# Optimization experiments

Hardware: AMD Instinct MI355X
Metric: run time of the kernel (lower is better)

The kernel has to match this reference:

```python
import jax, jax.numpy as jnp
import numpy as np

N_NODES = 50000


def setup_inputs() -> dict:
    key = jax.random.key(0)
    ks = jax.random.split(key, 10)
    B, N, D, H, O = 2, N_NODES, 128, 128, 10
    x = jax.random.normal(ks[0], (B, N, D), dtype=jnp.float32)
    edge_index = jax.random.randint(ks[1], (2, 800000), 0, N, dtype=jnp.int32)
    s = lambda fan_in: 1.0 / np.sqrt(fan_in)
    W  = jax.random.uniform(ks[2], (D, H), jnp.float32, -s(D), s(D))
    b  = jnp.zeros((H,), jnp.float32)
    W1 = jax.random.uniform(ks[3], (H, H // 2), jnp.float32, -s(H), s(H))
    b1 = jnp.zeros((H // 2,), jnp.float32)
    W2 = jax.random.uniform(ks[4], (H // 2, H // 4), jnp.float32, -s(H // 2), s(H // 2))
    b2 = jnp.zeros((H // 4,), jnp.float32)
    W3 = jax.random.uniform(ks[5], (H // 4, O), jnp.float32, -s(H // 4), s(H // 4))
    b3 = jnp.zeros((O,), jnp.float32)
    return {"x": x, "edge_index": edge_index, "W": W, "b": b,
            "W1": W1, "b1": b1, "W2": W2, "b2": b2, "W3": W3, "b3": b3}


def reference(x, edge_index, W, b, W1, b1, W2, b2, W3, b3):
    # GraphConvolution (Kipf): support = x @ W; out[dst] += support[src]; + b
    src, dst = edge_index[0], edge_index[1]
    support = jnp.einsum("bnd,dh->bnh", x, W)          # [B, N, H]
    msgs = support[:, src, :]                            # [B, E, H] gather
    agg = jnp.zeros_like(support).at[:, dst, :].add(msgs)  # scatter-add
    h = jax.nn.gelu(agg + b, approximate=False)          # GELU (torch default erf)
    # dropout is identity at inference (training=False)
    h = jax.nn.relu(jnp.einsum("bnh,hk->bnk", h, W1) + b1)
    h = jax.nn.relu(jnp.einsum("bnk,km->bnm", h, W2) + b2)
    h = jnp.einsum("bnm,mo->bno", h, W3) + b3            # [B, N, O]
    return h.mean(axis=1)                                # [B, O]
```

## Files before the change

kernel.cpp:

```cpp
#include <hip/hip_runtime.h>
#include <math.h>

#define NN 50000
#define DD 128
#define HH 128
#define L1 64
#define L2 32
#define OO 10

typedef short v8s __attribute__((ext_vector_type(8)));
typedef float v4f __attribute__((ext_vector_type(4)));

__device__ __forceinline__ float bf2f_lo(unsigned u) { return __uint_as_float(u << 16); }
__device__ __forceinline__ float bf2f_hi(unsigned u) { return __uint_as_float(u & 0xffff0000u); }
__device__ __forceinline__ unsigned short f2bf(float f) {
    unsigned u = __float_as_uint(f);
    return (unsigned short)((u + 0x7fffu + ((u >> 16) & 1u)) >> 16);
}
__device__ __forceinline__ float gelu_f(float v) {
    return 0.5f * v * (1.f + erff(v * 0.70710678118654752f));
}

__global__ __launch_bounds__(256) void k_wprep(
    const float* __restrict__ W, unsigned short* __restrict__ wtb)
{
    int i = blockIdx.x * 256 + threadIdx.x;
    if (i < 128 * 136) {
        int n = i / 136, k = i % 136;
        wtb[i] = (k < DD) ? f2bf(W[k * HH + n]) : (unsigned short)0;
    }
}

__global__ __launch_bounds__(256) void k_support(
    const float* __restrict__ x, const unsigned short* __restrict__ wtb,
    unsigned short* __restrict__ supb, int rows,
    const int* __restrict__ ei, int* __restrict__ counts, int E)
{
    __shared__ __align__(16) unsigned short xs[64 * 136];
    __shared__ __align__(16) unsigned short wt[128 * 136];
    const int tid = threadIdx.x;
    const int row0 = blockIdx.x * 64;

    for (int u = tid * 4; u < 128 * 136; u += 1024)
        *(uint2*)(&wt[u]) = *(const uint2*)(wtb + u);
    for (int u = tid * 4; u < 64 * DD; u += 1024) {
        const int r = u >> 7, c = u & 127;
        float4 v = make_float4(0.f, 0.f, 0.f, 0.f);
        if (row0 + r < rows) v = *(const float4*)(x + (size_t)(row0 + r) * DD + c);
        ushort4 o;
        o.x = f2bf(v.x); o.y = f2bf(v.y); o.z = f2bf(v.z); o.w = f2bf(v.w);
        *(ushort4*)(&xs[r * 136 + c]) = o;
    }

    {
        const int chunk = (E + gridDim.x - 1) / gridDim.x;
        const int e0 = blockIdx.x * chunk;
        const int e1 = min(e0 + chunk, E);
        for (int e = e0 + tid; e < e1; e += 256)
            atomicAdd(&counts[ei[(size_t)E + e]], 1);
    }
    __syncthreads();

    const int lane = tid & 63;
    const int w = tid >> 6;
    const int m0 = w * 16;
    const int lm = lane & 15;
    const int q  = lane >> 4;

    v4f acc[8];
    #pragma unroll
    for (int i = 0; i < 8; ++i) acc[i] = (v4f)(0.f);

    #pragma unroll
    for (int ks = 0; ks < 4; ++ks) {
        const int k0 = ks * 32 + q * 8;
        const v8s af = *(const v8s*)(&xs[(m0 + lm) * 136 + k0]);
        #pragma unroll
        for (int ct = 0; ct < 8; ++ct) {
            const v8s bf = *(const v8s*)(&wt[(ct * 16 + lm) * 136 + k0]);
            acc[ct] = __builtin_amdgcn_mfma_f32_16x16x32_bf16(af, bf, acc[ct], 0, 0, 0);
        }
    }

    #pragma unroll
    for (int ct = 0; ct < 8; ++ct) {
        const int col = ct * 16 + lm;
        #pragma unroll
        for (int r = 0; r < 4; ++r) {
            const int rowg = row0 + m0 + q * 4 + r;
            if (rowg < rows) {
                const int b = (rowg >= NN) ? 1 : 0;
                const int n = rowg - b * NN;
                supb[((size_t)n * 2 + b) * HH + col] = f2bf(acc[ct][r]);
            }
        }
    }
}

__global__ __launch_bounds__(1024) void k_scan1(
    const int* __restrict__ counts, int* __restrict__ offsets,
    int* __restrict__ blksum, int n)
{
    __shared__ int wsum[16], woff[16];
    const int tid = threadIdx.x, lane = tid & 63, wv = tid >> 6;
    const int i = blockIdx.x * 1024 + tid;
    int v = (i < n) ? counts[i] : 0;
    int x = v;
    #pragma unroll
    for (int d = 1; d < 64; d <<= 1) { int t = __shfl_up(x, d); if (lane >= d) x += t; }
    if (lane == 63) wsum[wv] = x;
    __syncthreads();
    if (wv == 0 && lane < 16) {
        int y = wsum[lane];
        #pragma unroll
        for (int d = 1; d < 16; d <<= 1) { int t = __shfl_up(y, d); if (lane >= d) y += t; }
        woff[lane] = y - wsum[lane];
        if (lane == 15) blksum[blockIdx.x] = y;
    }
    __syncthreads();
    if (i < n) offsets[i] = woff[wv] + (x - v);
}

__global__ __launch_bounds__(1024) void k_scan2(
    int* __restrict__ offsets, const int* __restrict__ blksum, int nblk, int n)
{
    __shared__ int base_sh, tot_sh;
    const int tid = threadIdx.x, lane = tid & 63, wv = tid >> 6;
    if (wv == 0) {
        int v = (lane < nblk) ? blksum[lane] : 0;
        int x = v;
        #pragma unroll
        for (int d = 1; d < 64; d <<= 1) { int t = __shfl_up(x, d); if (lane >= d) x += t; }
        int incl = __shfl(x, blockIdx.x);
        int own  = __shfl(v, blockIdx.x);
        int tot  = __shfl(x, nblk - 1);
        if (lane == 0) { base_sh = incl - own; tot_sh = tot; }
    }
    __syncthreads();
    const int i = blockIdx.x * 1024 + tid;
    if (i < n) offsets[i] += base_sh;
    if (blockIdx.x == nblk - 1 && tid == 0) offsets[n] = tot_sh;
}

__global__ __launch_bounds__(256) void k_bucket(
    const int* __restrict__ ei, const int* __restrict__ offsets,
    int* __restrict__ cursor, int* __restrict__ ss, int E)
{
    int e = blockIdx.x * 256 + threadIdx.x;
    if (e < E) {
        int d = ei[E + e];
        int pos = offsets[d] + atomicAdd(&cursor[d], 1);
        ss[pos] = ei[e];
    }
}

__global__ __launch_bounds__(256) void k_agg(
    const unsigned short* __restrict__ supb, const int* __restrict__ offsets,
    const int* __restrict__ ss, unsigned short* __restrict__ aggb, int nn)
{
    const int tid = threadIdx.x;
    const int lane = tid & 63;
    const int wv = tid >> 6;
    const int d = blockIdx.x * 4 + wv;
    if (d >= nn) return;
    const unsigned short* sp = supb + lane * 4;
    const int s0 = offsets[d], s1 = offsets[d + 1];
    float4 a = make_float4(0.f, 0.f, 0.f, 0.f);
    float4 a2 = make_float4(0.f, 0.f, 0.f, 0.f);
    int i = s0;
    for (; i + 4 <= s1; i += 4) {
        const int sA = ss[i], sB = ss[i + 1], sC = ss[i + 2], sD = ss[i + 3];
        const uint2 rA = *(const uint2*)(sp + (size_t)sA * 256);
        const uint2 rB = *(const uint2*)(sp + (size_t)sB * 256);
        const uint2 rC = *(const uint2*)(sp + (size_t)sC * 256);
        const uint2 rD = *(const uint2*)(sp + (size_t)sD * 256);
        a.x  += bf2f_lo(rA.x); a.y  += bf2f_hi(rA.x); a.z  += bf2f_lo(rA.y); a.w  += bf2f_hi(rA.y);
        a2.x += bf2f_lo(rB.x); a2.y += bf2f_hi(rB.x); a2.z += bf2f_lo(rB.y); a2.w += bf2f_hi(rB.y);
        a.x  += bf2f_lo(rC.x); a.y  += bf2f_hi(rC.x); a.z  += bf2f_lo(rC.y); a.w  += bf2f_hi(rC.y);
        a2.x += bf2f_lo(rD.x); a2.y += bf2f_hi(rD.x); a2.z += bf2f_lo(rD.y); a2.w += bf2f_hi(rD.y);
    }
    for (; i < s1; ++i) {
        const uint2 r = *(const uint2*)(sp + (size_t)ss[i] * 256);
        a.x += bf2f_lo(r.x); a.y += bf2f_hi(r.x); a.z += bf2f_lo(r.y); a.w += bf2f_hi(r.y);
    }
    a.x += a2.x; a.y += a2.y; a.z += a2.z; a.w += a2.w;
    ushort4 o;
    o.x = f2bf(a.x); o.y = f2bf(a.y); o.z = f2bf(a.z); o.w = f2bf(a.w);
    *(ushort4*)(aggb + (size_t)d * 256 + lane * 4) = o;
}

__global__ __launch_bounds__(512) void k_mlp(
    const unsigned short* __restrict__ aggb, const float* __restrict__ b0v,
    const float* __restrict__ W1, const float* __restrict__ b1v,
    const float* __restrict__ W2, const float* __restrict__ b2v,
    float* __restrict__ partials, int srows)
{
    __shared__ float w1s[HH][L1];
    __shared__ float w2s[L1][L2];
    __shared__ float hs[64 * 136];
    __shared__ float b0s[DD], b1s[L1], b2s[L2];
    __shared__ float oacc[64];

    const int tid = threadIdx.x;
    const int row0 = blockIdx.x * 64;

    for (int u = tid * 4; u < HH * L1; u += 2048)
        *(float4*)(&w1s[u >> 6][u & 63]) = *(const float4*)(W1 + u);
    for (int u = tid * 4; u < L1 * L2; u += 2048)
        *(float4*)(&w2s[u >> 5][u & 31]) = *(const float4*)(W2 + u);
    if (tid < DD) b0s[tid] = b0v[tid];
    if (tid < L1) b1s[tid] = b1v[tid];
    if (tid < L2) b2s[tid] = b2v[tid];
    if (tid < 64) oacc[tid] = 0.f;
    __syncthreads();

    for (int u = tid * 8; u < 64 * DD; u += 512 * 8) {
        const int r = u >> 7, c = u & 127;
        float4 g0 = make_float4(0.f, 0.f, 0.f, 0.f);
        float4 g1 = g0;
        if (row0 + r < srows) {
            const uint4 raw = *(const uint4*)(aggb + (size_t)(row0 + r) * HH + c);
            float v[8];
            v[0] = bf2f_lo(raw.x) + b0s[c + 0]; v[1] = bf2f_hi(raw.x) + b0s[c + 1];
            v[2] = bf2f_lo(raw.y) + b0s[c + 2]; v[3] = bf2f_hi(raw.y) + b0s[c + 3];
            v[4] = bf2f_lo(raw.z) + b0s[c + 4]; v[5] = bf2f_hi(raw.z) + b0s[c + 5];
            v[6] = bf2f_lo(raw.w) + b0s[c + 6]; v[7] = bf2f_hi(raw.w) + b0s[c + 7];
            #pragma unroll
            for (int t = 0; t < 8; ++t) v[t] = gelu_f(v[t]);
            g0 = make_float4(v[0], v[1], v[2], v[3]);
            g1 = make_float4(v[4], v[5], v[6], v[7]);
        }
        *(float4*)(&hs[r * 136 + c]) = g0;
        *(float4*)(&hs[r * 136 + c + 4]) = g1;
    }
    __syncthreads();

    const int cg = tid & 15;
    const int rg = tid >> 4;
    float4 acc0 = *(const float4*)(&b1s[cg * 4]);
    float4 acc1 = acc0;
    #pragma unroll 4
    for (int j = 0; j < HH; j += 4) {
        float4 wv[4];
        #pragma unroll
        for (int jj = 0; jj < 4; ++jj) wv[jj] = *(const float4*)(&w1s[j + jj][cg * 4]);
        const float4 h0 = *(const float4*)(&hs[(rg * 2 + 0) * 136 + j]);
        const float4 h1 = *(const float4*)(&hs[(rg * 2 + 1) * 136 + j]);
        acc0.x = fmaf(h0.x, wv[0].x, fmaf(h0.y, wv[1].x, fmaf(h0.z, wv[2].x, fmaf(h0.w, wv[3].x, acc0.x))));
        acc0.y = fmaf(h0.x, wv[0].y, fmaf(h0.y, wv[1].y, fmaf(h0.z, wv[2].y, fmaf(h0.w, wv[3].y, acc0.y))));
        acc0.z = fmaf(h0.x, wv[0].z, fmaf(h0.y, wv[1].z, fmaf(h0.z, wv[2].z, fmaf(h0.w, wv[3].z, acc0.z))));
        acc0.w = fmaf(h0.x, wv[0].w, fmaf(h0.y, wv[1].w, fmaf(h0.z, wv[2].w, fmaf(h0.w, wv[3].w, acc0.w))));
        acc1.x = fmaf(h1.x, wv[0].x, fmaf(h1.y, wv[1].x, fmaf(h1.z, wv[2].x, fmaf(h1.w, wv[3].x, acc1.x))));
        acc1.y = fmaf(h1.x, wv[0].y, fmaf(h1.y, wv[1].y, fmaf(h1.z, wv[2].y, fmaf(h1.w, wv[3].y, acc1.y))));
        acc1.z = fmaf(h1.x, wv[0].z, fmaf(h1.y, wv[1].z, fmaf(h1.z, wv[2].z, fmaf(h1.w, wv[3].z, acc1.z))));
        acc1.w = fmaf(h1.x, wv[0].w, fmaf(h1.y, wv[1].w, fmaf(h1.z, wv[2].w, fmaf(h1.w, wv[3].w, acc1.w))));
    }
    acc0.x = fmaxf(acc0.x, 0.f); acc0.y = fmaxf(acc0.y, 0.f);
    acc0.z = fmaxf(acc0.z, 0.f); acc0.w = fmaxf(acc0.w, 0.f);
    acc1.x = fmaxf(acc1.x, 0.f); acc1.y = fmaxf(acc1.y, 0.f);
    acc1.z = fmaxf(acc1.z, 0.f); acc1.w = fmaxf(acc1.w, 0.f);
    __syncthreads();
    float* h1p = hs;
    *(float4*)(&h1p[(rg * 2 + 0) * 68 + cg * 4]) = acc0;
    *(float4*)(&h1p[(rg * 2 + 1) * 68 + cg * 4]) = acc1;
    __syncthreads();

    float* h2p = hs + 5120;
    {
        const int cg2 = tid & 7;
        const int r2 = tid >> 3;
        float4 a = *(const float4*)(&b2s[cg2 * 4]);
        #pragma unroll 4
        for (int j = 0; j < L1; j += 4) {
            float4 wv[4];
            #pragma unroll
            for (int jj = 0; jj < 4; ++jj) wv[jj] = *(const float4*)(&w2s[j + jj][cg2 * 4]);
            const float4 hv = *(const float4*)(&h1p[r2 * 68 + j]);
            a.x = fmaf(hv.x, wv[0].x, fmaf(hv.y, wv[1].x, fmaf(hv.z, wv[2].x, fmaf(hv.w, wv[3].x, a.x))));
            a.y = fmaf(hv.x, wv[0].y, fmaf(hv.y, wv[1].y, fmaf(hv.z, wv[2].y, fmaf(hv.w, wv[3].y, a.y))));
            a.z = fmaf(hv.x, wv[0].z, fmaf(hv.y, wv[1].z, fmaf(hv.z, wv[2].z, fmaf(hv.w, wv[3].z, a.z))));
            a.w = fmaf(hv.x, wv[0].w, fmaf(hv.y, wv[1].w, fmaf(hv.z, wv[2].w, fmaf(hv.w, wv[3].w, a.w))));
        }
        a.x = fmaxf(a.x, 0.f); a.y = fmaxf(a.y, 0.f);
        a.z = fmaxf(a.z, 0.f); a.w = fmaxf(a.w, 0.f);
        __syncthreads();
        *(float4*)(&h2p[r2 * 36 + cg2 * 4]) = a;
    }
    __syncthreads();

    {
        const int c = tid & 31;
        const int g = tid >> 5;
        float p0 = 0.f, p1 = 0.f;
        #pragma unroll
        for (int i = 0; i < 4; ++i) {
            const int r = g * 4 + i;
            if (row0 + r < srows) {
                const float v = h2p[r * 36 + c];
                if (r & 1) p1 += v; else p0 += v;
            }
        }
        if (p0 != 0.f) atomicAdd(&oacc[c], p0);
        if (p1 != 0.f) atomicAdd(&oacc[32 + c], p1);
    }
    __syncthreads();
    if (tid < 64) partials[(size_t)blockIdx.x * 64 + tid] = oacc[tid];
}

__global__ __launch_bounds__(256) void k_scatter(
    const int* __restrict__ ei, const unsigned short* __restrict__ supb,
    float* __restrict__ aggf, int E)
{
    const int tid = threadIdx.x;
    const int eg = tid >> 6;
    const int lane = tid & 63;
    const int e = blockIdx.x * 4 + eg;
    if (e >= E) return;
    const int src = ei[e];
    const int dst = ei[E + e];
    const uint2 r = *(const uint2*)(supb + (size_t)src * 256 + lane * 4);
    float* ap = aggf + (size_t)dst * 256 + lane * 4;
    unsafeAtomicAdd(ap + 0, bf2f_lo(r.x));
    unsafeAtomicAdd(ap + 1, bf2f_hi(r.x));
    unsafeAtomicAdd(ap + 2, bf2f_lo(r.y));
    unsafeAtomicAdd(ap + 3, bf2f_hi(r.y));
}

__global__ __launch_bounds__(256) void k_cvt(
    const float* __restrict__ in, unsigned short* __restrict__ outb, int n)
{
    int i = blockIdx.x * 256 + threadIdx.x;
    if (i < n) outb[i] = f2bf(in[i]);
}

__global__ __launch_bounds__(256) void k_reduce(
    const float* __restrict__ partials, float* __restrict__ accum, int nblk)
{
    __shared__ float lsum[4][64];
    const int t = threadIdx.x & 63;
    const int w = threadIdx.x >> 6;
    float s = 0.f;
    for (int g = blockIdx.x * 4 + w; g < nblk; g += gridDim.x * 4)
        s += partials[(size_t)g * 64 + t];
    lsum[w][t] = s;
    __syncthreads();
    if (threadIdx.x < 64) {
        const float v = lsum[0][t] + lsum[1][t] + lsum[2][t] + lsum[3][t];
        unsafeAtomicAdd(&accum[t], v);
    }
}

__global__ __launch_bounds__(64) void k_final(
    const float* __restrict__ accum, const float* __restrict__ W3,
    const float* __restrict__ b3v, float* __restrict__ out)
{
    const int tid = threadIdx.x;
    if (tid < 2 * OO) {
        const int b = tid / OO, o = tid % OO;
        float acc = b3v[o];
        const float inv = 1.0f / (float)NN;
        #pragma unroll
        for (int j = 0; j < L2; ++j) acc += (accum[b * 32 + j] * inv) * W3[j * OO + o];
        out[tid] = acc;
    }
}

extern "C" void kernel_launch(void* const* d_in, const int* in_sizes, int n_in,
                              void* d_out, int out_size, void* d_ws, size_t ws_size,
                              hipStream_t stream) {
    const float* x  = (const float*)d_in[0];
    const int*   ei = (const int*)d_in[1];
    const float* W  = (const float*)d_in[2];
    const float* b0 = (const float*)d_in[3];
    const float* W1 = (const float*)d_in[4];
    const float* b1 = (const float*)d_in[5];
    const float* W2 = (const float*)d_in[6];
    const float* b2 = (const float*)d_in[7];
    const float* W3 = (const float*)d_in[8];
    const float* b3 = (const float*)d_in[9];
    float* out = (float*)d_out;

    const int E = in_sizes[1] / 2;
    const int rows = 2 * NN;
    const int nblk = (rows + 63) / 64;
    const int nsb = (NN + 1023) / 1024;

    unsigned short* supb = (unsigned short*)d_ws;
    unsigned short* aggb = supb + (size_t)rows * HH;
    float* partials = (float*)(aggb + (size_t)rows * HH);
    float* accum    = partials + (size_t)nblk * 64;
    int*   counts   = (int*)(accum + 64);
    int*   cursor   = counts + NN;
    int*   offsets  = cursor + NN;
    int*   blksum   = offsets + NN + 1;
    unsigned short* wtb = (unsigned short*)(blksum + 64);
    int*   ss       = (int*)(wtb + 128 * 136);
    float* aggf     = (float*)(ss + E);
    const size_t need_csr = ((size_t)rows * HH * 2 + 128 * 136) * sizeof(unsigned short)
                      + ((size_t)nblk * 64 + 64) * sizeof(float)
                      + ((size_t)NN * 3 + 1 + 64 + E) * sizeof(int);
    const size_t need_fb = need_csr + (size_t)rows * HH * sizeof(float);

    if (ws_size >= need_csr && nsb <= 64) {
        hipMemsetAsync(accum, 0, (64 + 2 * (size_t)NN) * sizeof(int), stream);
        k_wprep<<<dim3((128 * 136 + 255) / 256), dim3(256), 0, stream>>>(W, wtb);
        k_support<<<dim3((rows + 63) / 64), dim3(256), 0, stream>>>(x, wtb, supb, rows, ei, counts, E);
        k_scan1<<<dim3(nsb), dim3(1024), 0, stream>>>(counts, offsets, blksum, NN);
        k_scan2<<<dim3(nsb), dim3(1024), 0, stream>>>(offsets, blksum, nsb, NN);
        k_bucket<<<dim3((E + 255) / 256), dim3(256), 0, stream>>>(ei, offsets, cursor, ss, E);
        k_agg<<<dim3((NN + 3) / 4), dim3(256), 0, stream>>>(supb, offsets, ss, aggb, NN);
        k_mlp<<<dim3(nblk), dim3(512), 0, stream>>>(aggb, b0, W1, b1, W2, b2, partials, rows);
    } else if (ws_size >= need_fb) {
        hipMemsetAsync(accum, 0, 64 * sizeof(float), stream);
        hipMemsetAsync(aggf, 0, (size_t)rows * HH * sizeof(float), stream);
        k_wprep<<<dim3((128 * 136 + 255) / 256), dim3(256), 0, stream>>>(W, wtb);
        k_support<<<dim3((rows + 63) / 64), dim3(256), 0, stream>>>(x, wtb, supb, rows, ei, counts, 0);
        k_scatter<<<dim3((E + 3) / 4), dim3(256), 0, stream>>>(ei, supb, aggf, E);
        k_cvt<<<dim3((rows * HH + 255) / 256), dim3(256), 0, stream>>>(aggf, aggb, rows * HH);
        k_mlp<<<dim3(nblk), dim3(512), 0, stream>>>(aggb, b0, W1, b1, W2, b2, partials, rows);
    }

    k_reduce<<<dim3(64), dim3(256), 0, stream>>>(partials, accum, nblk);
    k_final<<<dim3(1), dim3(64), 0, stream>>>(accum, W3, b3, out);
}
```

Before: 310.2 us.

## Use bf16 MFMA for MLP layers and enlarge support-GEMM tiles

The two MLP layers (128→64, 64→32) in k_mlp now run on bf16 MFMA instructions instead of scalar fp32 FMAs. The weights are pre-transposed and converted to bf16 in k_wprep, and the GELU activations and layer-1 outputs are stored as bf16 in shared memory. Separately, k_support now uses 128-row tiles with 512 threads, so each block amortises the shared weight load over more rows. This adds bf16 rounding of the intermediate activations and weights, and the larger support tile uses more LDS per block, which may lower occupancy.

```diff
diff --git a/kernel.cpp b/kernel.cpp
--- a/kernel.cpp
+++ b/kernel.cpp
@@ -22,28 +22,38 @@
 }
 
 __global__ __launch_bounds__(256) void k_wprep(
-    const float* __restrict__ W, unsigned short* __restrict__ wtb)
+    const float* __restrict__ W, const float* __restrict__ W1,
+    const float* __restrict__ W2, unsigned short* __restrict__ wtb,
+    unsigned short* __restrict__ w1tb, unsigned short* __restrict__ w2tb)
 {
     int i = blockIdx.x * 256 + threadIdx.x;
     if (i < 128 * 136) {
         int n = i / 136, k = i % 136;
         wtb[i] = (k < DD) ? f2bf(W[k * HH + n]) : (unsigned short)0;
-    }
-}
-
-__global__ __launch_bounds__(256) void k_support(
+    } else if (i < 128 * 136 + 64 * 136) {
+        int j = i - 128 * 136;
+        int n = j / 136, k = j % 136;
+        w1tb[j] = (k < HH) ? f2bf(W1[k * L1 + n]) : (unsigned short)0;
+    } else if (i < 128 * 136 + 64 * 136 + 32 * 72) {
+        int j = i - (128 * 136 + 64 * 136);
+        int n = j / 72, k = j % 72;
+        w2tb[j] = (k < L1) ? f2bf(W2[k * L2 + n]) : (unsigned short)0;
+    }
+}
+
+__global__ __launch_bounds__(512, 4) void k_support(
     const float* __restrict__ x, const unsigned short* __restrict__ wtb,
     unsigned short* __restrict__ supb, int rows,
     const int* __restrict__ ei, int* __restrict__ counts, int E)
 {
-    __shared__ __align__(16) unsigned short xs[64 * 136];
+    __shared__ __align__(16) unsigned short xs[128 * 136];
     __shared__ __align__(16) unsigned short wt[128 * 136];
     const int tid = threadIdx.x;
-    const int row0 = blockIdx.x * 64;
-
-    for (int u = tid * 4; u < 128 * 136; u += 1024)
+    const int row0 = blockIdx.x * 128;
+
+    for (int u = tid * 4; u < 128 * 136; u += 2048)
         *(uint2*)(&wt[u]) = *(const uint2*)(wtb + u);
-    for (int u = tid * 4; u < 64 * DD; u += 1024) {
+    for (int u = tid * 4; u < 128 * DD; u += 2048) {
         const int r = u >> 7, c = u & 127;
         float4 v = make_float4(0.f, 0.f, 0.f, 0.f);
         if (row0 + r < rows) v = *(const float4*)(x + (size_t)(row0 + r) * DD + c);
@@ -56,7 +66,7 @@
         const int chunk = (E + gridDim.x - 1) / gridDim.x;
         const int e0 = blockIdx.x * chunk;
         const int e1 = min(e0 + chunk, E);
-        for (int e = e0 + tid; e < e1; e += 256)
+        for (int e = e0 + tid; e < e1; e += 512)
             atomicAdd(&counts[ei[(size_t)E + e]], 1);
     }
     __syncthreads();
@@ -189,102 +199,98 @@
     *(ushort4*)(aggb + (size_t)d * 256 + lane * 4) = o;
 }
 
-__global__ __launch_bounds__(512) void k_mlp(
+__global__ __launch_bounds__(512, 6) void k_mlp(
     const unsigned short* __restrict__ aggb, const float* __restrict__ b0v,
-    const float* __restrict__ W1, const float* __restrict__ b1v,
-    const float* __restrict__ W2, const float* __restrict__ b2v,
+    const unsigned short* __restrict__ w1tb, const float* __restrict__ b1v,
+    const unsigned short* __restrict__ w2tb, const float* __restrict__ b2v,
     float* __restrict__ partials, int srows)
 {
-    __shared__ float w1s[HH][L1];
-    __shared__ float w2s[L1][L2];
-    __shared__ float hs[64 * 136];
+    __shared__ __align__(16) unsigned short wt1[64 * 136];
+    __shared__ __align__(16) unsigned short wt2[32 * 72];
+    __shared__ __align__(16) unsigned char upool[64 * 136 * 2];
+    __shared__ __align__(16) unsigned short h1b[64 * 72];
     __shared__ float b0s[DD], b1s[L1], b2s[L2];
     __shared__ float oacc[64];
+    unsigned short* hsb = (unsigned short*)upool;
+    float* h2p = (float*)upool;
 
     const int tid = threadIdx.x;
     const int row0 = blockIdx.x * 64;
 
-    for (int u = tid * 4; u < HH * L1; u += 2048)
-        *(float4*)(&w1s[u >> 6][u & 63]) = *(const float4*)(W1 + u);
-    for (int u = tid * 4; u < L1 * L2; u += 2048)
-        *(float4*)(&w2s[u >> 5][u & 31]) = *(const float4*)(W2 + u);
+    for (int u = tid * 4; u < 64 * 136; u += 2048)
+        *(uint2*)(&wt1[u]) = *(const uint2*)(w1tb + u);
+    for (int u = tid * 4; u < 32 * 72; u += 2048)
+        *(uint2*)(&wt2[u]) = *(const uint2*)(w2tb + u);
     if (tid < DD) b0s[tid] = b0v[tid];
     if (tid < L1) b1s[tid] = b1v[tid];
     if (tid < L2) b2s[tid] = b2v[tid];
     if (tid < 64) oacc[tid] = 0.f;
-    __syncthreads();
-
-    for (int u = tid * 8; u < 64 * DD; u += 512 * 8) {
+
+    for (int u = tid * 8; u < 64 * DD; u += 4096) {
         const int r = u >> 7, c = u & 127;
-        float4 g0 = make_float4(0.f, 0.f, 0.f, 0.f);
-        float4 g1 = g0;
-        if (row0 + r < srows) {
-            const uint4 raw = *(const uint4*)(aggb + (size_t)(row0 + r) * HH + c);
-            float v[8];
-            v[0] = bf2f_lo(raw.x) + b0s[c + 0]; v[1] = bf2f_hi(raw.x) + b0s[c + 1];
-            v[2] = bf2f_lo(raw.y) + b0s[c + 2]; v[3] = bf2f_hi(raw.y) + b0s[c + 3];
-            v[4] = bf2f_lo(raw.z) + b0s[c + 4]; v[5] = bf2f_hi(raw.z) + b0s[c + 5];
-            v[6] = bf2f_lo(raw.w) + b0s[c + 6]; v[7] = bf2f_hi(raw.w) + b0s[c + 7];
+        uint4 raw = make_uint4(0, 0, 0, 0);
+        if (row0 + r < srows) raw = *(const uint4*)(aggb + (size_t)(row0 + r) * HH + c);
+        float v[8];
+        v[0] = bf2f_lo(raw.x) + b0s[c + 0]; v[1] = bf2f_hi(raw.x) + b0s[c + 1];
+        v[2] = bf2f_lo(raw.y) + b0s[c + 2]; v[3] = bf2f_hi(raw.y) + b0s[c + 3];
+        v[4] = bf2f_lo(raw.z) + b0s[c + 4]; v[5] = bf2f_hi(raw.z) + b0s[c + 5];
+        v[6] = bf2f_lo(raw.w) + b0s[c + 6]; v[7] = bf2f_hi(raw.w) + b0s[c + 7];
+        ushort4 o0, o1;
+        o0.x = f2bf(gelu_f(v[0])); o0.y = f2bf(gelu_f(v[1]));
+        o0.z = f2bf(gelu_f(v[2])); o0.w = f2bf(gelu_f(v[3]));
+        o1.x = f2bf(gelu_f(v[4])); o1.y = f2bf(gelu_f(v[5]));
+        o1.z = f2bf(gelu_f(v[6])); o1.w = f2bf(gelu_f(v[7]));
+        *(ushort4*)(&hsb[r * 136 + c]) = o0;
+        *(ushort4*)(&hsb[r * 136 + c + 4]) = o1;
+    }
+    __syncthreads();
+
+    const int lane = tid & 63;
+    const int w = tid >> 6;
+    const int lm = lane & 15;
+    const int q = lane >> 4;
+    const int r1 = (w & 3) * 16;
+
+    {
+        const int c1 = (w >> 2) * 32;
+        v4f a1[2];
+        a1[0] = (v4f)(0.f); a1[1] = (v4f)(0.f);
+        #pragma unroll
+        for (int ks = 0; ks < 4; ++ks) {
+            const int k0 = ks * 32 + q * 8;
+            const v8s af = *(const v8s*)(&hsb[(r1 + lm) * 136 + k0]);
             #pragma unroll
-            for (int t = 0; t < 8; ++t) v[t] = gelu_f(v[t]);
-            g0 = make_float4(v[0], v[1], v[2], v[3]);
-            g1 = make_float4(v[4], v[5], v[6], v[7]);
-        }
-        *(float4*)(&hs[r * 136 + c]) = g0;
-        *(float4*)(&hs[r * 136 + c + 4]) = g1;
-    }
-    __syncthreads();
-
-    const int cg = tid & 15;
-    const int rg = tid >> 4;
-    float4 acc0 = *(const float4*)(&b1s[cg * 4]);
-    float4 acc1 = acc0;
-    #pragma unroll 4
-    for (int j = 0; j < HH; j += 4) {
-        float4 wv[4];
-        #pragma unroll
-        for (int jj = 0; jj < 4; ++jj) wv[jj] = *(const float4*)(&w1s[j + jj][cg * 4]);
-        const float4 h0 = *(const float4*)(&hs[(rg * 2 + 0) * 136 + j]);
-        const float4 h1 = *(const float4*)(&hs[(rg * 2 + 1) * 136 + j]);
-        acc0.x = fmaf(h0.x, wv[0].x, fmaf(h0.y, wv[1].x, fmaf(h0.z, wv[2].x, fmaf(h0.w, wv[3].x, acc0.x))));
-        acc0.y = fmaf(h0.x, wv[0].y, fmaf(h0.y, wv[1].y, fmaf(h0.z, wv[2].y, fmaf(h0.w, wv[3].y, acc0.y))));
-        acc0.z = fmaf(h0.x, wv[0].z, fmaf(h0.y, wv[1].z, fmaf(h0.z, wv[2].z, fmaf(h0.w, wv[3].z, acc0.z))));
-        acc0.w = fmaf(h0.x, wv[0].w, fmaf(h0.y, wv[1].w, fmaf(h0.z, wv[2].w, fmaf(h0.w, wv[3].w, acc0.w))));
-        acc1.x = fmaf(h1.x, wv[0].x, fmaf(h1.y, wv[1].x, fmaf(h1.z, wv[2].x, fmaf(h1.w, wv[3].x, acc1.x))));
-        acc1.y = fmaf(h1.x, wv[0].y, fmaf(h1.y, wv[1].y, fmaf(h1.z, wv[2].y, fmaf(h1.w, wv[3].y, acc1.y))));
-        acc1.z = fmaf(h1.x, wv[0].z, fmaf(h1.y, wv[1].z, fmaf(h1.z, wv[2].z, fmaf(h1.w, wv[3].z, acc1.z))));
-        acc1.w = fmaf(h1.x, wv[0].w, fmaf(h1.y, wv[1].w, fmaf(h1.z, wv[2].w, fmaf(h1.w, wv[3].w, acc1.w))));
-    }
-    acc0.x = fmaxf(acc0.x, 0.f); acc0.y = fmaxf(acc0.y, 0.f);
-    acc0.z = fmaxf(acc0.z, 0.f); acc0.w = fmaxf(acc0.w, 0.f);
-    acc1.x = fmaxf(acc1.x, 0.f); acc1.y = fmaxf(acc1.y, 0.f);
-    acc1.z = fmaxf(acc1.z, 0.f); acc1.w = fmaxf(acc1.w, 0.f);
-    __syncthreads();
-    float* h1p = hs;
-    *(float4*)(&h1p[(rg * 2 + 0) * 68 + cg * 4]) = acc0;
-    *(float4*)(&h1p[(rg * 2 + 1) * 68 + cg * 4]) = acc1;
-    __syncthreads();
-
-    float* h2p = hs + 5120;
+            for (int ct = 0; ct < 2; ++ct) {
+                const v8s bf = *(const v8s*)(&wt1[(c1 + ct * 16 + lm) * 136 + k0]);
+                a1[ct] = __builtin_amdgcn_mfma_f32_16x16x32_bf16(af, bf, a1[ct], 0, 0, 0);
+            }
+        }
+        #pragma unroll
+        for (int ct = 0; ct < 2; ++ct) {
+            const int col = c1 + ct * 16 + lm;
+            const float bias = b1s[col];
+            #pragma unroll
+            for (int r = 0; r < 4; ++r)
+                h1b[(r1 + q * 4 + r) * 72 + col] = f2bf(fmaxf(a1[ct][r] + bias, 0.f));
+        }
+    }
+    __syncthreads();
+
     {
-        const int cg2 = tid & 7;
-        const int r2 = tid >> 3;
-        float4 a = *(const float4*)(&b2s[cg2 * 4]);
-        #pragma unroll 4
-        for (int j = 0; j < L1; j += 4) {
-            float4 wv[4];
-            #pragma unroll
-            for (int jj = 0; jj < 4; ++jj) wv[jj] = *(const float4*)(&w2s[j + jj][cg2 * 4]);
-            const float4 hv = *(const float4*)(&h1p[r2 * 68 + j]);
-            a.x = fmaf(hv.x, wv[0].x, fmaf(hv.y, wv[1].x, fmaf(hv.z, wv[2].x, fmaf(hv.w, wv[3].x, a.x))));
-            a.y = fmaf(hv.x, wv[0].y, fmaf(hv.y, wv[1].y, fmaf(hv.z, wv[2].y, fmaf(hv.w, wv[3].y, a.y))));
-            a.z = fmaf(hv.x, wv[0].z, fmaf(hv.y, wv[1].z, fmaf(hv.z, wv[2].z, fmaf(hv.w, wv[3].z, a.z))));
-            a.w = fmaf(hv.x, wv[0].w, fmaf(hv.y, wv[1].w, fmaf(hv.z, wv[2].w, fmaf(hv.w, wv[3].w, a.w))));
-        }
-        a.x = fmaxf(a.x, 0.f); a.y = fmaxf(a.y, 0.f);
-        a.z = fmaxf(a.z, 0.f); a.w = fmaxf(a.w, 0.f);
-        __syncthreads();
-        *(float4*)(&h2p[r2 * 36 + cg2 * 4]) = a;
+        const int c2 = (w >> 2) * 16;
+        v4f a2 = (v4f)(0.f);
+        #pragma unroll
+        for (int ks = 0; ks < 2; ++ks) {
+            const int k0 = ks * 32 + q * 8;
+            const v8s af = *(const v8s*)(&h1b[(r1 + lm) * 72 + k0]);
+            const v8s bf = *(const v8s*)(&wt2[(c2 + lm) * 72 + k0]);
+            a2 = __builtin_amdgcn_mfma_f32_16x16x32_bf16(af, bf, a2, 0, 0, 0);
+        }
+        const int col = c2 + lm;
+        const float bias = b2s[col];
+        #pragma unroll
+        for (int r = 0; r < 4; ++r)
+            h2p[(r1 + q * 4 + r) * 36 + col] = fmaxf(a2[r] + bias, 0.f);
     }
     __syncthreads();
 
@@ -384,6 +390,7 @@
     const int rows = 2 * NN;
     const int nblk = (rows + 63) / 64;
     const int nsb = (NN + 1023) / 1024;
+    const int wpn = 128 * 136 + 64 * 136 + 32 * 72;
 
     unsigned short* supb = (unsigned short*)d_ws;
     unsigned short* aggb = supb + (size_t)rows * HH;
@@ -393,31 +400,33 @@
     int*   cursor   = counts + NN;
     int*   offsets  = cursor + NN;
     int*   blksum   = offsets + NN + 1;
-    unsigned short* wtb = (unsigned short*)(blksum + 64);
-    int*   ss       = (int*)(wtb + 128 * 136);
+    unsigned short* wtb  = (unsigned short*)(blksum + 64);
+    unsigned short* w1tb = wtb + 128 * 136;
+    unsigned short* w2tb = w1tb + 64 * 136;
+    int*   ss       = (int*)(w2tb + 32 * 72);
     float* aggf     = (float*)(ss + E);
-    const size_t need_csr = ((size_t)rows * HH * 2 + 128 * 136) * sizeof(unsigned short)
+    const size_t need_csr = ((size_t)rows * HH * 2 + wpn) * sizeof(unsigned short)
                       + ((size_t)nblk * 64 + 64) * sizeof(float)
                       + ((size_t)NN * 3 + 1 + 64 + E) * sizeof(int);
     const size_t need_fb = need_csr + (size_t)rows * HH * sizeof(float);
 
     if (ws_size >= need_csr && nsb <= 64) {
         hipMemsetAsync(accum, 0, (64 + 2 * (size_t)NN) * sizeof(int), stream);
-        k_wprep<<<dim3((128 * 136 + 255) / 256), dim3(256), 0, stream>>>(W, wtb);
-        k_support<<<dim3((rows + 63) / 64), dim3(256), 0, stream>>>(x, wtb, supb, rows, ei, counts, E);
+        k_wprep<<<dim3((wpn + 255) / 256), dim3(256), 0, stream>>>(W, W1, W2, wtb, w1tb, w2tb);
+        k_support<<<dim3((rows + 127) / 128), dim3(512), 0, stream>>>(x, wtb, supb, rows, ei, counts, E);
         k_scan1<<<dim3(nsb), dim3(1024), 0, stream>>>(counts, offsets, blksum, NN);
         k_scan2<<<dim3(nsb), dim3(1024), 0, stream>>>(offsets, blksum, nsb, NN);
         k_bucket<<<dim3((E + 255) / 256), dim3(256), 0, stream>>>(ei, offsets, cursor, ss, E);
         k_agg<<<dim3((NN + 3) / 4), dim3(256), 0, stream>>>(supb, offsets, ss, aggb, NN);
-        k_mlp<<<dim3(nblk), dim3(512), 0, stream>>>(aggb, b0, W1, b1, W2, b2, partials, rows);
+        k_mlp<<<dim3(nblk), dim3(512), 0, stream>>>(aggb, b0, w1tb, b1, w2tb, b2, partials, rows);
     } else if (ws_size >= need_fb) {
         hipMemsetAsync(accum, 0, 64 * sizeof(float), stream);
         hipMemsetAsync(aggf, 0, (size_t)rows * HH * sizeof(float), stream);
-        k_wprep<<<dim3((128 * 136 + 255) / 256), dim3(256), 0, stream>>>(W, wtb);
-        k_support<<<dim3((rows + 63) / 64), dim3(256), 0, stream>>>(x, wtb, supb, rows, ei, counts, 0);
+        k_wprep<<<dim3((wpn + 255) / 256), dim3(256), 0, stream>>>(W, W1, W2, wtb, w1tb, w2tb);
+        k_support<<<dim3((rows + 127) / 128), dim3(512), 0, stream>>>(x, wtb, supb, rows, ei, counts, 0);
         k_scatter<<<dim3((E + 3) / 4), dim3(256), 0, stream>>>(ei, supb, aggf, E);
         k_cvt<<<dim3((rows * HH + 255) / 256), dim3(256), 0, stream>>>(aggf, aggb, rows * HH);
-        k_mlp<<<dim3(nblk), dim3(512), 0, stream>>>(aggb, b0, W1, b1, W2, b2, partials, rows);
+        k_mlp<<<dim3(nblk), dim3(512), 0, stream>>>(aggb, b0, w1tb, b1, w2tb, b2, partials, rows);
     }
 
     k_reduce<<<dim3(64), dim3(256), 0, stream>>>(partials, accum, nblk);
```

Result: faster. 274.0 us (-11.7%).
